# Optimization experiments

Hardware: AMD Instinct MI355X
Metric: run time of the kernel (lower is better)

Reference implementation:

```python
import jax, jax.numpy as jnp
import numpy as np

N_NODES = 50000
N_EDGES = 500000
D_MODEL = 256
N_HEADS = 8
D_K = D_MODEL // N_HEADS


def setup_inputs() -> dict:
    key = jax.random.key(0)
    ks = jax.random.split(key, 12)
    s = 1.0 / np.sqrt(D_MODEL)
    inp = {
        "query": jax.random.normal(ks[0], (N_NODES, D_MODEL), dtype=jnp.float32),
        "key": jax.random.normal(ks[1], (N_NODES, D_MODEL), dtype=jnp.float32),
        "value": jax.random.normal(ks[2], (N_NODES, D_MODEL), dtype=jnp.float32),
        "edges": jax.random.randint(ks[3], (2, N_EDGES), 0, N_NODES, dtype=jnp.int64),
        # four nn.Linear(d_model, d_model) layers: q, k, v, out
        "Wq": jax.random.uniform(ks[4], (D_MODEL, D_MODEL), jnp.float32, -s, s),
        "bq": jax.random.uniform(ks[5], (D_MODEL,), jnp.float32, -s, s),
        "Wk": jax.random.uniform(ks[6], (D_MODEL, D_MODEL), jnp.float32, -s, s),
        "bk": jax.random.uniform(ks[7], (D_MODEL,), jnp.float32, -s, s),
        "Wv": jax.random.uniform(ks[8], (D_MODEL, D_MODEL), jnp.float32, -s, s),
        "bv": jax.random.uniform(ks[9], (D_MODEL,), jnp.float32, -s, s),
        "Wo": jax.random.uniform(ks[10], (D_MODEL, D_MODEL), jnp.float32, -s, s),
        "bo": jax.random.uniform(ks[11], (D_MODEL,), jnp.float32, -s, s),
    }
    return inp


def reference(query, key, value, edges, Wq, bq, Wk, bk, Wv, bv, Wo, bo):
    N = query.shape[0]
    # linear projections (torch Linear: x @ W.T + b), view as [N, h, d_k]
    q = (query @ Wq.T + bq).reshape(N, N_HEADS, D_K)
    k = (key @ Wk.T + bk).reshape(N, N_HEADS, D_K)
    v = (value @ Wv.T + bv).reshape(N, N_HEADS, D_K)

    dst, src = edges[0], edges[1]
    # per-edge dot-product scores [E, h]
    scores = jnp.einsum("ehd,ehd->eh", q[dst], k[src]) / jnp.sqrt(
        jnp.asarray(D_K, dtype=q.dtype)
    )
    # segment softmax over destination node neighborhoods (per head)
    m = jax.ops.segment_max(scores, dst, num_segments=N)  # [N, h]
    ex = jnp.exp(scores - m[dst])
    den = jax.ops.segment_sum(ex, dst, num_segments=N)  # [N, h]
    p_attn = ex / den[dst]  # [E, h]

    # weighted scatter-sum of gathered values -> [N, h, d_k]
    out = jax.ops.segment_sum(p_attn[:, :, None] * v[src], dst, num_segments=N)
    out = out.reshape(N, D_MODEL)
    return out @ Wo.T + bo
```

## Files before the change

### kernel.cpp

```cpp
#include <hip/hip_runtime.h>
#include <hip/hip_bf16.h>
#include <cstdint>

#define D_MODEL 256
#define NHEADS 8
#define DK 32
#define LDSPAD 8
#define LDSROW (D_MODEL + LDSPAD)
#define LDSROWF (D_MODEL + 4)
#define PBLK 170

typedef float f32x4 __attribute__((ext_vector_type(4)));
typedef __bf16 bf16x8 __attribute__((ext_vector_type(8)));
typedef unsigned short u16x8 __attribute__((ext_vector_type(8)));

__device__ __forceinline__ unsigned short f2bf_rne(float f) {
    unsigned int u = __float_as_uint(f);
    u += 0x7FFF + ((u >> 16) & 1);
    return (unsigned short)(u >> 16);
}
__device__ __forceinline__ float bf2f(unsigned short h) {
    return __uint_as_float(((unsigned int)h) << 16);
}

__global__ void conv_weights_hist(const float* __restrict__ W0, const float* __restrict__ W1,
                                  const float* __restrict__ W2, const float* __restrict__ W3,
                                  unsigned short* __restrict__ out,
                                  const int* __restrict__ dst, int E,
                                  int* __restrict__ counts) {
    int i = blockIdx.x * blockDim.x + threadIdx.x;
    if (i < 4 * 8192) {
        const int w    = i >> 13;
        const int rem  = i & 8191;
        const int lane = rem & 63;
        const int kk   = (rem >> 6) & 7;
        const int ntile= rem >> 9;
        const int row  = ntile * 16 + (lane & 15);
        const int col  = kk * 32 + (lane >> 4) * 8;
        const float* Wsrc = (w == 0) ? W0 : (w == 1) ? W1 : (w == 2) ? W2 : W3;
        const float* sp = Wsrc + (size_t)row * D_MODEL + col;
        float4 x0 = *(const float4*)sp;
        float4 x1 = *(const float4*)(sp + 4);
        unsigned short* dp = out + (size_t)w * D_MODEL * D_MODEL + (size_t)rem * 8;
        ushort4 o0, o1;
        o0.x = f2bf_rne(x0.x); o0.y = f2bf_rne(x0.y); o0.z = f2bf_rne(x0.z); o0.w = f2bf_rne(x0.w);
        o1.x = f2bf_rne(x1.x); o1.y = f2bf_rne(x1.y); o1.z = f2bf_rne(x1.z); o1.w = f2bf_rne(x1.w);
        *(ushort4*)dp = o0;
        *(ushort4*)(dp + 4) = o1;
    } else {
        const int e = i - 4 * 8192;
        if (e < E) atomicAdd(&counts[dst[e]], 1);
    }
}

__global__ __launch_bounds__(256, 2) void gemm_qkv(
    const float* __restrict__ Aq, const float* __restrict__ Ak, const float* __restrict__ Av,
    const unsigned short* __restrict__ Wsw,
    const float* __restrict__ bq, const float* __restrict__ bk, const float* __restrict__ bv,
    unsigned short* __restrict__ qbuf, unsigned short* __restrict__ kvbuf,
    int M, int mtiles)
{
    __shared__ __align__(16) unsigned short smem[32 * LDSROW];

    const int which = blockIdx.y;
    const float* A = (which == 0) ? Aq : (which == 1) ? Ak : Av;
    const float* bias = (which == 0) ? bq : (which == 1) ? bk : bv;
    const unsigned short* Wb = Wsw + (size_t)which * D_MODEL * D_MODEL;
    unsigned short* outp = (which == 0) ? qbuf : kvbuf;
    const int voff = (which == 2) ? 4 : 0;

    const int lane  = threadIdx.x & 63;
    const int wave  = threadIdx.x >> 6;
    const int mrow  = lane & 15;
    const int quad  = lane >> 4;

    bf16x8 bfr[4][8];
#pragma unroll
    for (int ni = 0; ni < 4; ++ni)
#pragma unroll
        for (int kk = 0; kk < 8; ++kk)
            bfr[ni][kk] = *(const bf16x8*)(Wb + ((size_t)((wave * 4 + ni) * 8 + kk) * 64 + lane) * 8);

    float bcol[4];
#pragma unroll
    for (int ni = 0; ni < 4; ++ni) bcol[ni] = bias[wave * 64 + ni * 16 + mrow];

    for (int t = blockIdx.x; t < mtiles; t += PBLK) {
        const int m0 = t * 32;

#pragma unroll
        for (int i = 0; i < 8; ++i) {
            const int g = i * 256 + threadIdx.x;
            const int r = g >> 6, c4 = g & 63;
            const int grow = min(m0 + r, M - 1);
            float4 x = *(const float4*)(A + (size_t)grow * D_MODEL + c4 * 4);
            ushort4 o;
            o.x = f2bf_rne(x.x); o.y = f2bf_rne(x.y);
            o.z = f2bf_rne(x.z); o.w = f2bf_rne(x.w);
            *(ushort4*)(smem + r * LDSROW + c4 * 4) = o;
        }
        __syncthreads();

        f32x4 acc[2][4] = {};
#pragma unroll
        for (int kk = 0; kk < 8; ++kk) {
            bf16x8 afr[2];
#pragma unroll
            for (int mi = 0; mi < 2; ++mi)
                afr[mi] = *(const bf16x8*)(smem + (mi * 16 + mrow) * LDSROW + kk * 32 + quad * 8);
#pragma unroll
            for (int mi = 0; mi < 2; ++mi)
#pragma unroll
                for (int ni = 0; ni < 4; ++ni)
                    acc[mi][ni] = __builtin_amdgcn_mfma_f32_16x16x32_bf16(
                        afr[mi], bfr[ni][kk], acc[mi][ni], 0, 0, 0);
        }

        __syncthreads();
#pragma unroll
        for (int ni = 0; ni < 4; ++ni) {
            const int col = wave * 64 + ni * 16 + mrow;
#pragma unroll
            for (int mi = 0; mi < 2; ++mi)
#pragma unroll
                for (int r = 0; r < 4; ++r)
                    smem[(mi * 16 + quad * 4 + r) * LDSROW + col] =
                        f2bf_rne(acc[mi][ni][r] + bcol[ni]);
        }
        __syncthreads();
#pragma unroll
        for (int i = 0; i < 4; ++i) {
            const int g = i * 256 + threadIdx.x;
            const int r = g >> 5, c8 = g & 31;
            const int grow = m0 + r;
            if (grow < M) {
                if (which == 0) {
                    bf16x8 x = *(const bf16x8*)(smem + r * LDSROW + c8 * 8);
                    *(bf16x8*)(outp + (size_t)grow * D_MODEL + c8 * 8) = x;
                } else {
                    ushort4 lo = *(const ushort4*)(smem + r * LDSROW + c8 * 8);
                    ushort4 hi = *(const ushort4*)(smem + r * LDSROW + c8 * 8 + 4);
                    unsigned short* base = outp + (size_t)grow * 512 + 16 * c8 + voff;
                    *(ushort4*)base = lo;
                    *(ushort4*)(base + 8) = hi;
                }
            }
        }
        __syncthreads();
    }
}

__global__ __launch_bounds__(256, 2) void gemm_out(
    const unsigned short* __restrict__ Ab, const unsigned short* __restrict__ Wb,
    const float* __restrict__ bias, float* __restrict__ outp, int M, int mtiles)
{
    __shared__ __align__(16) char smem_raw[32 * LDSROWF * 4];
    unsigned short* smemA = (unsigned short*)smem_raw;
    float*          smemF = (float*)smem_raw;

    const int lane  = threadIdx.x & 63;
    const int wave  = threadIdx.x >> 6;
    const int mrow  = lane & 15;
    const int quad  = lane >> 4;

    bf16x8 bfr[4][8];
#pragma unroll
    for (int ni = 0; ni < 4; ++ni)
#pragma unroll
        for (int kk = 0; kk < 8; ++kk)
            bfr[ni][kk] = *(const bf16x8*)(Wb + ((size_t)((wave * 4 + ni) * 8 + kk) * 64 + lane) * 8);

    float bcol[4];
#pragma unroll
    for (int ni = 0; ni < 4; ++ni) bcol[ni] = bias[wave * 64 + ni * 16 + mrow];

    for (int t = blockIdx.x; t < mtiles; t += 3 * PBLK) {
        const int m0 = t * 32;

#pragma unroll
        for (int i = 0; i < 4; ++i) {
            const int g = i * 256 + threadIdx.x;
            const int r = g >> 5, c8 = g & 31;
            const int grow = min(m0 + r, M - 1);
            bf16x8 x = *(const bf16x8*)(Ab + (size_t)grow * D_MODEL + c8 * 8);
            *(bf16x8*)(smemA + r * LDSROW + c8 * 8) = x;
        }
        __syncthreads();

        f32x4 acc[2][4] = {};
#pragma unroll
        for (int kk = 0; kk < 8; ++kk) {
            bf16x8 afr[2];
#pragma unroll
            for (int mi = 0; mi < 2; ++mi)
                afr[mi] = *(const bf16x8*)(smemA + (mi * 16 + mrow) * LDSROW + kk * 32 + quad * 8);
#pragma unroll
            for (int mi = 0; mi < 2; ++mi)
#pragma unroll
                for (int ni = 0; ni < 4; ++ni)
                    acc[mi][ni] = __builtin_amdgcn_mfma_f32_16x16x32_bf16(
                        afr[mi], bfr[ni][kk], acc[mi][ni], 0, 0, 0);
        }

        __syncthreads();
#pragma unroll
        for (int ni = 0; ni < 4; ++ni) {
            const int col = wave * 64 + ni * 16 + mrow;
#pragma unroll
            for (int mi = 0; mi < 2; ++mi)
#pragma unroll
                for (int r = 0; r < 4; ++r)
                    smemF[(mi * 16 + quad * 4 + r) * LDSROWF + col] = acc[mi][ni][r] + bcol[ni];
        }
        __syncthreads();
#pragma unroll
        for (int i = 0; i < 8; ++i) {
            const int g = i * 256 + threadIdx.x;
            const int r = g >> 6, c4 = g & 63;
            const int grow = m0 + r;
            if (grow < M) {
                float4 x = *(const float4*)(smemF + r * LDSROWF + c4 * 4);
                *(float4*)(outp + (size_t)grow * D_MODEL + c4 * 4) = x;
            }
        }
        __syncthreads();
    }
}

__global__ void block_reduce_kernel(const int* __restrict__ counts, int N,
                                    int* __restrict__ blockSums) {
    const int g = blockIdx.x * 256 + threadIdx.x;
    int v = (g < N) ? counts[g] : 0;
#pragma unroll
    for (int d = 1; d < 64; d <<= 1) v += __shfl_xor(v, d);
    __shared__ int ws[4];
    if ((threadIdx.x & 63) == 0) ws[threadIdx.x >> 6] = v;
    __syncthreads();
    if (threadIdx.x == 0) blockSums[blockIdx.x] = ws[0] + ws[1] + ws[2] + ws[3];
}

__global__ void scan_blocks_kernel(int* __restrict__ blockSums, int G) {
    __shared__ int sh[256];
    const int t = threadIdx.x;
    int v = (t < G) ? blockSums[t] : 0;
    sh[t] = v;
    __syncthreads();
#pragma unroll
    for (int off = 1; off < 256; off <<= 1) {
        int add = (t >= off) ? sh[t - off] : 0;
        __syncthreads();
        sh[t] += add;
        __syncthreads();
    }
    if (t < G) blockSums[t] = sh[t] - v;
}

__global__ void scan_write_kernel(const int* __restrict__ counts, int N,
                                  const int* __restrict__ blockOffsets,
                                  int* __restrict__ offsets) {
    const int g = blockIdx.x * 256 + threadIdx.x;
    const int t = threadIdx.x;
    int v = (g < N) ? counts[g] : 0;
    __shared__ int sh[256];
    sh[t] = v;
    __syncthreads();
#pragma unroll
    for (int off = 1; off < 256; off <<= 1) {
        int add = (t >= off) ? sh[t - off] : 0;
        __syncthreads();
        sh[t] += add;
        __syncthreads();
    }
    if (g <= N) offsets[g] = sh[t] - v + blockOffsets[blockIdx.x];
}

__global__ void fill_kernel(const int* __restrict__ dst, const int* __restrict__ src, int E,
                            const int* __restrict__ offsets, int* __restrict__ cursor,
                            int* __restrict__ ssrc) {
    int i = blockIdx.x * blockDim.x + threadIdx.x;
    if (i < E) {
        int d = dst[i];
        int r = atomicAdd(&cursor[d], 1);
        ssrc[offsets[d] + r] = src[i];
    }
}

__global__ __launch_bounds__(256) void attn_kernel(
    const unsigned short* __restrict__ qb, const unsigned short* __restrict__ kv,
    const int* __restrict__ offsets, const int* __restrict__ ssrc,
    unsigned short* __restrict__ attn, int N)
{
    const int node = blockIdx.x * 4 + (threadIdx.x >> 6);
    if (node >= N) return;
    const int lane = threadIdx.x & 63;

    ushort4 qu = *(const ushort4*)(qb + (size_t)node * D_MODEL + 4 * lane);
    const float sc = 0.17677669529663689f;
    float qx = bf2f(qu.x) * sc, qy = bf2f(qu.y) * sc,
          qz = bf2f(qu.z) * sc, qw = bf2f(qu.w) * sc;

    float m = -INFINITY, l = 0.f;
    float ax = 0.f, ay = 0.f, az = 0.f, aw = 0.f;

    const int e0 = offsets[node], e1 = offsets[node + 1];
    int e = e0;

    for (; e + 7 < e1; e += 8) {
        u16x8 a0 = *(const u16x8*)(kv + (size_t)ssrc[e]     * 512 + 8 * lane);
        u16x8 a1 = *(const u16x8*)(kv + (size_t)ssrc[e + 1] * 512 + 8 * lane);
        u16x8 a2 = *(const u16x8*)(kv + (size_t)ssrc[e + 2] * 512 + 8 * lane);
        u16x8 a3 = *(const u16x8*)(kv + (size_t)ssrc[e + 3] * 512 + 8 * lane);
        u16x8 a4 = *(const u16x8*)(kv + (size_t)ssrc[e + 4] * 512 + 8 * lane);
        u16x8 a5 = *(const u16x8*)(kv + (size_t)ssrc[e + 5] * 512 + 8 * lane);
        u16x8 a6 = *(const u16x8*)(kv + (size_t)ssrc[e + 6] * 512 + 8 * lane);
        u16x8 a7 = *(const u16x8*)(kv + (size_t)ssrc[e + 7] * 512 + 8 * lane);

        float p0 = qx * bf2f(a0[0]) + qy * bf2f(a0[1]) + qz * bf2f(a0[2]) + qw * bf2f(a0[3]);
        float p1 = qx * bf2f(a1[0]) + qy * bf2f(a1[1]) + qz * bf2f(a1[2]) + qw * bf2f(a1[3]);
        float p2 = qx * bf2f(a2[0]) + qy * bf2f(a2[1]) + qz * bf2f(a2[2]) + qw * bf2f(a2[3]);
        float p3 = qx * bf2f(a3[0]) + qy * bf2f(a3[1]) + qz * bf2f(a3[2]) + qw * bf2f(a3[3]);
        float p4 = qx * bf2f(a4[0]) + qy * bf2f(a4[1]) + qz * bf2f(a4[2]) + qw * bf2f(a4[3]);
        float p5 = qx * bf2f(a5[0]) + qy * bf2f(a5[1]) + qz * bf2f(a5[2]) + qw * bf2f(a5[3]);
        float p6 = qx * bf2f(a6[0]) + qy * bf2f(a6[1]) + qz * bf2f(a6[2]) + qw * bf2f(a6[3]);
        float p7 = qx * bf2f(a7[0]) + qy * bf2f(a7[1]) + qz * bf2f(a7[2]) + qw * bf2f(a7[3]);
#pragma unroll
        for (int d = 1; d <= 4; d <<= 1) {
            p0 += __shfl_xor(p0, d); p1 += __shfl_xor(p1, d);
            p2 += __shfl_xor(p2, d); p3 += __shfl_xor(p3, d);
            p4 += __shfl_xor(p4, d); p5 += __shfl_xor(p5, d);
            p6 += __shfl_xor(p6, d); p7 += __shfl_xor(p7, d);
        }
        float mnew = fmaxf(fmaxf(fmaxf(fmaxf(m, p0), fmaxf(p1, p2)), fmaxf(fmaxf(p3, p4), fmaxf(p5, p6))), p7);
        float alpha = __expf(m - mnew);
        float w0 = __expf(p0 - mnew), w1 = __expf(p1 - mnew);
        float w2 = __expf(p2 - mnew), w3 = __expf(p3 - mnew);
        float w4 = __expf(p4 - mnew), w5 = __expf(p5 - mnew);
        float w6 = __expf(p6 - mnew), w7 = __expf(p7 - mnew);
        ax = ax * alpha + w0 * bf2f(a0[4]) + w1 * bf2f(a1[4]) + w2 * bf2f(a2[4]) + w3 * bf2f(a3[4])
                        + w4 * bf2f(a4[4]) + w5 * bf2f(a5[4]) + w6 * bf2f(a6[4]) + w7 * bf2f(a7[4]);
        ay = ay * alpha + w0 * bf2f(a0[5]) + w1 * bf2f(a1[5]) + w2 * bf2f(a2[5]) + w3 * bf2f(a3[5])
                        + w4 * bf2f(a4[5]) + w5 * bf2f(a5[5]) + w6 * bf2f(a6[5]) + w7 * bf2f(a7[5]);
        az = az * alpha + w0 * bf2f(a0[6]) + w1 * bf2f(a1[6]) + w2 * bf2f(a2[6]) + w3 * bf2f(a3[6])
                        + w4 * bf2f(a4[6]) + w5 * bf2f(a5[6]) + w6 * bf2f(a6[6]) + w7 * bf2f(a7[6]);
        aw = aw * alpha + w0 * bf2f(a0[7]) + w1 * bf2f(a1[7]) + w2 * bf2f(a2[7]) + w3 * bf2f(a3[7])
                        + w4 * bf2f(a4[7]) + w5 * bf2f(a5[7]) + w6 * bf2f(a6[7]) + w7 * bf2f(a7[7]);
        l = l * alpha + w0 + w1 + w2 + w3 + w4 + w5 + w6 + w7;
        m = mnew;
    }

    for (; e + 3 < e1; e += 4) {
        u16x8 a0 = *(const u16x8*)(kv + (size_t)ssrc[e]     * 512 + 8 * lane);
        u16x8 a1 = *(const u16x8*)(kv + (size_t)ssrc[e + 1] * 512 + 8 * lane);
        u16x8 a2 = *(const u16x8*)(kv + (size_t)ssrc[e + 2] * 512 + 8 * lane);
        u16x8 a3 = *(const u16x8*)(kv + (size_t)ssrc[e + 3] * 512 + 8 * lane);

        float p0 = qx * bf2f(a0[0]) + qy * bf2f(a0[1]) + qz * bf2f(a0[2]) + qw * bf2f(a0[3]);
        float p1 = qx * bf2f(a1[0]) + qy * bf2f(a1[1]) + qz * bf2f(a1[2]) + qw * bf2f(a1[3]);
        float p2 = qx * bf2f(a2[0]) + qy * bf2f(a2[1]) + qz * bf2f(a2[2]) + qw * bf2f(a2[3]);
        float p3 = qx * bf2f(a3[0]) + qy * bf2f(a3[1]) + qz * bf2f(a3[2]) + qw * bf2f(a3[3]);
#pragma unroll
        for (int d = 1; d <= 4; d <<= 1) {
            p0 += __shfl_xor(p0, d); p1 += __shfl_xor(p1, d);
            p2 += __shfl_xor(p2, d); p3 += __shfl_xor(p3, d);
        }
        float mnew = fmaxf(fmaxf(fmaxf(m, p0), fmaxf(p1, p2)), p3);
        float alpha = __expf(m - mnew);
        float w0 = __expf(p0 - mnew), w1 = __expf(p1 - mnew);
        float w2 = __expf(p2 - mnew), w3 = __expf(p3 - mnew);
        ax = ax * alpha + w0 * bf2f(a0[4]) + w1 * bf2f(a1[4]) + w2 * bf2f(a2[4]) + w3 * bf2f(a3[4]);
        ay = ay * alpha + w0 * bf2f(a0[5]) + w1 * bf2f(a1[5]) + w2 * bf2f(a2[5]) + w3 * bf2f(a3[5]);
        az = az * alpha + w0 * bf2f(a0[6]) + w1 * bf2f(a1[6]) + w2 * bf2f(a2[6]) + w3 * bf2f(a3[6]);
        aw = aw * alpha + w0 * bf2f(a0[7]) + w1 * bf2f(a1[7]) + w2 * bf2f(a2[7]) + w3 * bf2f(a3[7]);
        l = l * alpha + w0 + w1 + w2 + w3;
        m = mnew;
    }

    for (; e < e1; ++e) {
        int s = ssrc[e];
        u16x8 a = *(const u16x8*)(kv + (size_t)s * 512 + 8 * lane);
        float p = qx * bf2f(a[0]) + qy * bf2f(a[1]) + qz * bf2f(a[2]) + qw * bf2f(a[3]);
        p += __shfl_xor(p, 1);
        p += __shfl_xor(p, 2);
        p += __shfl_xor(p, 4);
        float mnew  = fmaxf(m, p);
        float alpha = __expf(m - mnew);
        float w     = __expf(p - mnew);
        ax = ax * alpha + w * bf2f(a[4]);
        ay = ay * alpha + w * bf2f(a[5]);
        az = az * alpha + w * bf2f(a[6]);
        aw = aw * alpha + w * bf2f(a[7]);
        l = l * alpha + w;
        m = mnew;
    }

    const float inv = (l > 0.f) ? 1.f / l : 0.f;
    ushort4 o;
    o.x = f2bf_rne(ax * inv);
    o.y = f2bf_rne(ay * inv);
    o.z = f2bf_rne(az * inv);
    o.w = f2bf_rne(aw * inv);
    *(ushort4*)(attn + (size_t)node * D_MODEL + 4 * lane) = o;
}

extern "C" void kernel_launch(void* const* d_in, const int* in_sizes, int n_in,
                              void* d_out, int out_size, void* d_ws, size_t ws_size,
                              hipStream_t stream)
{
    const float* query = (const float*)d_in[0];
    const float* key   = (const float*)d_in[1];
    const float* value = (const float*)d_in[2];
    const int*   edges = (const int*)d_in[3];
    const float* Wq = (const float*)d_in[4];
    const float* bq = (const float*)d_in[5];
    const float* Wk = (const float*)d_in[6];
    const float* bk = (const float*)d_in[7];
    const float* Wv = (const float*)d_in[8];
    const float* bv = (const float*)d_in[9];
    const float* Wo = (const float*)d_in[10];
    const float* bo = (const float*)d_in[11];
    float* out = (float*)d_out;

    const int N = in_sizes[0] / D_MODEL;
    const int E = in_sizes[3] / 2;
    const int* dst = edges;
    const int* src = edges + E;

    char* ws = (char*)d_ws;
    size_t off = 0;
    auto alloc = [&](size_t bytes) {
        void* p = ws + off;
        off += (bytes + 255) & ~(size_t)255;
        return p;
    };
    unsigned short* qbuf  = (unsigned short*)alloc((size_t)N * D_MODEL * 2);
    unsigned short* kvbuf = (unsigned short*)alloc((size_t)N * 2 * D_MODEL * 2);
    unsigned short* attnb = (unsigned short*)alloc((size_t)N * D_MODEL * 2);
    unsigned short* Wbuf  = (unsigned short*)alloc((size_t)4 * D_MODEL * D_MODEL * 2);
    int*            counts  = (int*)alloc((size_t)2 * N * 4);
    int*            offsets = (int*)alloc((size_t)(N + 1) * 4);
    int*            ssrc    = (int*)alloc((size_t)E * 4);
    int*            bsums   = (int*)alloc((size_t)256 * 4);

    hipMemsetAsync(counts, 0, (size_t)2 * N * 4, stream);

    const int fused_threads = 4 * 8192 + E;
    conv_weights_hist<<<(fused_threads + 255) / 256, 256, 0, stream>>>(
        Wq, Wk, Wv, Wo, Wbuf, dst, E, counts);

    const int mtiles = (N + 31) / 32;
    gemm_qkv<<<dim3(PBLK, 3), 256, 0, stream>>>(query, key, value, Wbuf,
                                                bq, bk, bv, qbuf, kvbuf, N, mtiles);

    const int G = (N + 256) / 256;
    block_reduce_kernel<<<G, 256, 0, stream>>>(counts, N, bsums);
    scan_blocks_kernel<<<1, 256, 0, stream>>>(bsums, G);
    scan_write_kernel<<<G, 256, 0, stream>>>(counts, N, bsums, offsets);

    const int eblocks = (E + 255) / 256;
    fill_kernel<<<eblocks, 256, 0, stream>>>(dst, src, E, offsets, counts + N, ssrc);
    attn_kernel<<<(N + 3) / 4, 256, 0, stream>>>(qbuf, kvbuf, offsets, ssrc, attnb, N);

    gemm_out<<<3 * PBLK, 256, 0, stream>>>(attnb, Wbuf + 3 * D_MODEL * D_MODEL, bo, out, N, mtiles);
}
```

Measured before the change: 369.6 us.

## Use 8-wave GEMM blocks and prefetch next A tile into registers

Both projection GEMMs now run 512-thread blocks, so each wave covers 32 output columns instead of 64. This halves the per-wave weight fragments held in registers and allows higher occupancy. The global loads for the next 32-row tile are issued into registers before the current tile's MFMA work, overlapping memory latency with compute. Grid sizes change to 168x3 and 512 blocks. In exchange, more waves redundantly read the same LDS A tile, and the prefetch registers add pressure.

```diff
diff --git a/kernel.cpp b/kernel.cpp
--- a/kernel.cpp
+++ b/kernel.cpp
@@ -8,7 +8,8 @@
 #define LDSPAD 8
 #define LDSROW (D_MODEL + LDSPAD)
 #define LDSROWF (D_MODEL + 4)
-#define PBLK 170
+#define QBLK 168
+#define OBLK 512
 
 typedef float f32x4 __attribute__((ext_vector_type(4)));
 typedef __bf16 bf16x8 __attribute__((ext_vector_type(8)));
@@ -53,7 +54,7 @@
     }
 }
 
-__global__ __launch_bounds__(256, 2) void gemm_qkv(
+__global__ __launch_bounds__(512, 4) void gemm_qkv(
     const float* __restrict__ Aq, const float* __restrict__ Ak, const float* __restrict__ Av,
     const unsigned short* __restrict__ Wsw,
     const float* __restrict__ bq, const float* __restrict__ bk, const float* __restrict__ bv,
@@ -74,34 +75,57 @@
     const int mrow  = lane & 15;
     const int quad  = lane >> 4;
 
-    bf16x8 bfr[4][8];
-#pragma unroll
-    for (int ni = 0; ni < 4; ++ni)
+    bf16x8 bfr[2][8];
+#pragma unroll
+    for (int ni = 0; ni < 2; ++ni)
 #pragma unroll
         for (int kk = 0; kk < 8; ++kk)
-            bfr[ni][kk] = *(const bf16x8*)(Wb + ((size_t)((wave * 4 + ni) * 8 + kk) * 64 + lane) * 8);
-
-    float bcol[4];
-#pragma unroll
-    for (int ni = 0; ni < 4; ++ni) bcol[ni] = bias[wave * 64 + ni * 16 + mrow];
-
-    for (int t = blockIdx.x; t < mtiles; t += PBLK) {
+            bfr[ni][kk] = *(const bf16x8*)(Wb + ((size_t)((wave * 2 + ni) * 8 + kk) * 64 + lane) * 8);
+
+    float bcol[2];
+#pragma unroll
+    for (int ni = 0; ni < 2; ++ni) bcol[ni] = bias[wave * 32 + ni * 16 + mrow];
+
+    int t = blockIdx.x;
+    float4 pf[4];
+    if (t < mtiles) {
         const int m0 = t * 32;
-
-#pragma unroll
-        for (int i = 0; i < 8; ++i) {
-            const int g = i * 256 + threadIdx.x;
+#pragma unroll
+        for (int i = 0; i < 4; ++i) {
+            const int g = i * 512 + threadIdx.x;
             const int r = g >> 6, c4 = g & 63;
             const int grow = min(m0 + r, M - 1);
-            float4 x = *(const float4*)(A + (size_t)grow * D_MODEL + c4 * 4);
+            pf[i] = *(const float4*)(A + (size_t)grow * D_MODEL + c4 * 4);
+        }
+    }
+
+    for (; t < mtiles; t += QBLK) {
+        const int m0 = t * 32;
+
+#pragma unroll
+        for (int i = 0; i < 4; ++i) {
+            const int g = i * 512 + threadIdx.x;
+            const int r = g >> 6, c4 = g & 63;
             ushort4 o;
-            o.x = f2bf_rne(x.x); o.y = f2bf_rne(x.y);
-            o.z = f2bf_rne(x.z); o.w = f2bf_rne(x.w);
+            o.x = f2bf_rne(pf[i].x); o.y = f2bf_rne(pf[i].y);
+            o.z = f2bf_rne(pf[i].z); o.w = f2bf_rne(pf[i].w);
             *(ushort4*)(smem + r * LDSROW + c4 * 4) = o;
         }
         __syncthreads();
 
-        f32x4 acc[2][4] = {};
+        const int tn = t + QBLK;
+        if (tn < mtiles) {
+            const int m0n = tn * 32;
+#pragma unroll
+            for (int i = 0; i < 4; ++i) {
+                const int g = i * 512 + threadIdx.x;
+                const int r = g >> 6, c4 = g & 63;
+                const int grow = min(m0n + r, M - 1);
+                pf[i] = *(const float4*)(A + (size_t)grow * D_MODEL + c4 * 4);
+            }
+        }
+
+        f32x4 acc[2][2] = {};
 #pragma unroll
         for (int kk = 0; kk < 8; ++kk) {
             bf16x8 afr[2];
@@ -111,15 +135,15 @@
 #pragma unroll
             for (int mi = 0; mi < 2; ++mi)
 #pragma unroll
-                for (int ni = 0; ni < 4; ++ni)
+                for (int ni = 0; ni < 2; ++ni)
                     acc[mi][ni] = __builtin_amdgcn_mfma_f32_16x16x32_bf16(
                         afr[mi], bfr[ni][kk], acc[mi][ni], 0, 0, 0);
         }
 
         __syncthreads();
 #pragma unroll
-        for (int ni = 0; ni < 4; ++ni) {
-            const int col = wave * 64 + ni * 16 + mrow;
+        for (int ni = 0; ni < 2; ++ni) {
+            const int col = wave * 32 + ni * 16 + mrow;
 #pragma unroll
             for (int mi = 0; mi < 2; ++mi)
 #pragma unroll
@@ -129,8 +153,8 @@
         }
         __syncthreads();
 #pragma unroll
-        for (int i = 0; i < 4; ++i) {
-            const int g = i * 256 + threadIdx.x;
+        for (int i = 0; i < 2; ++i) {
+            const int g = i * 512 + threadIdx.x;
             const int r = g >> 5, c8 = g & 31;
             const int grow = m0 + r;
             if (grow < M) {
@@ -150,7 +174,7 @@
     }
 }
 
-__global__ __launch_bounds__(256, 2) void gemm_out(
+__global__ __launch_bounds__(512, 4) void gemm_out(
     const unsigned short* __restrict__ Ab, const unsigned short* __restrict__ Wb,
     const float* __restrict__ bias, float* __restrict__ outp, int M, int mtiles)
 {
@@ -163,31 +187,54 @@
     const int mrow  = lane & 15;
     const int quad  = lane >> 4;
 
-    bf16x8 bfr[4][8];
-#pragma unroll
-    for (int ni = 0; ni < 4; ++ni)
+    bf16x8 bfr[2][8];
+#pragma unroll
+    for (int ni = 0; ni < 2; ++ni)
 #pragma unroll
         for (int kk = 0; kk < 8; ++kk)
-            bfr[ni][kk] = *(const bf16x8*)(Wb + ((size_t)((wave * 4 + ni) * 8 + kk) * 64 + lane) * 8);
-
-    float bcol[4];
-#pragma unroll
-    for (int ni = 0; ni < 4; ++ni) bcol[ni] = bias[wave * 64 + ni * 16 + mrow];
-
-    for (int t = blockIdx.x; t < mtiles; t += 3 * PBLK) {
+            bfr[ni][kk] = *(const bf16x8*)(Wb + ((size_t)((wave * 2 + ni) * 8 + kk) * 64 + lane) * 8);
+
+    float bcol[2];
+#pragma unroll
+    for (int ni = 0; ni < 2; ++ni) bcol[ni] = bias[wave * 32 + ni * 16 + mrow];
+
+    int t = blockIdx.x;
+    bf16x8 pf[2];
+    if (t < mtiles) {
         const int m0 = t * 32;
-
-#pragma unroll
-        for (int i = 0; i < 4; ++i) {
-            const int g = i * 256 + threadIdx.x;
+#pragma unroll
+        for (int i = 0; i < 2; ++i) {
+            const int g = i * 512 + threadIdx.x;
             const int r = g >> 5, c8 = g & 31;
             const int grow = min(m0 + r, M - 1);
-            bf16x8 x = *(const bf16x8*)(Ab + (size_t)grow * D_MODEL + c8 * 8);
-            *(bf16x8*)(smemA + r * LDSROW + c8 * 8) = x;
-        }
-        __syncthreads();
-
-        f32x4 acc[2][4] = {};
+            pf[i] = *(const bf16x8*)(Ab + (size_t)grow * D_MODEL + c8 * 8);
+        }
+    }
+
+    for (; t < mtiles; t += OBLK) {
+        const int m0 = t * 32;
+
+#pragma unroll
+        for (int i = 0; i < 2; ++i) {
+            const int g = i * 512 + threadIdx.x;
+            const int r = g >> 5, c8 = g & 31;
+            *(bf16x8*)(smemA + r * LDSROW + c8 * 8) = pf[i];
+        }
+        __syncthreads();
+
+        const int tn = t + OBLK;
+        if (tn < mtiles) {
+            const int m0n = tn * 32;
+#pragma unroll
+            for (int i = 0; i < 2; ++i) {
+                const int g = i * 512 + threadIdx.x;
+                const int r = g >> 5, c8 = g & 31;
+                const int grow = min(m0n + r, M - 1);
+                pf[i] = *(const bf16x8*)(Ab + (size_t)grow * D_MODEL + c8 * 8);
+            }
+        }
+
+        f32x4 acc[2][2] = {};
 #pragma unroll
         for (int kk = 0; kk < 8; ++kk) {
             bf16x8 afr[2];
@@ -197,15 +244,15 @@
 #pragma unroll
             for (int mi = 0; mi < 2; ++mi)
 #pragma unroll
-                for (int ni = 0; ni < 4; ++ni)
+                for (int ni = 0; ni < 2; ++ni)
                     acc[mi][ni] = __builtin_amdgcn_mfma_f32_16x16x32_bf16(
                         afr[mi], bfr[ni][kk], acc[mi][ni], 0, 0, 0);
         }
 
         __syncthreads();
 #pragma unroll
-        for (int ni = 0; ni < 4; ++ni) {
-            const int col = wave * 64 + ni * 16 + mrow;
+        for (int ni = 0; ni < 2; ++ni) {
+            const int col = wave * 32 + ni * 16 + mrow;
 #pragma unroll
             for (int mi = 0; mi < 2; ++mi)
 #pragma unroll
@@ -214,8 +261,8 @@
         }
         __syncthreads();
 #pragma unroll
-        for (int i = 0; i < 8; ++i) {
-            const int g = i * 256 + threadIdx.x;
+        for (int i = 0; i < 4; ++i) {
+            const int g = i * 512 + threadIdx.x;
             const int r = g >> 6, c4 = g & 63;
             const int grow = m0 + r;
             if (grow < M) {
@@ -448,7 +495,7 @@
         Wq, Wk, Wv, Wo, Wbuf, dst, E, counts);
 
     const int mtiles = (N + 31) / 32;
-    gemm_qkv<<<dim3(PBLK, 3), 256, 0, stream>>>(query, key, value, Wbuf,
+    gemm_qkv<<<dim3(QBLK, 3), 512, 0, stream>>>(query, key, value, Wbuf,
                                                 bq, bk, bv, qbuf, kvbuf, N, mtiles);
 
     const int G = (N + 256) / 256;
@@ -460,5 +507,5 @@
     fill_kernel<<<eblocks, 256, 0, stream>>>(dst, src, E, offsets, counts + N, ssrc);
     attn_kernel<<<(N + 3) / 4, 256, 0, stream>>>(qbuf, kvbuf, offsets, ssrc, attnb, N);
 
-    gemm_out<<<3 * PBLK, 256, 0, stream>>>(attnb, Wbuf + 3 * D_MODEL * D_MODEL, bo, out, N, mtiles);
-}
+    gemm_out<<<OBLK, 512, 0, stream>>>(attnb, Wbuf + 3 * D_MODEL * D_MODEL, bo, out, N, mtiles);
+}
```

New measurement: 366.4 us. About the same (-0.9%).
